# Optimization experiments

Hardware: AMD Instinct MI355X
Metric: run time of the kernel (lower is better)

Reference implementation:

```python
import jax, jax.numpy as jnp
import numpy as np

K = 3
TAPS = K ** 3  # 27 taps of the 3x3x3 kernel


def _conv3d(x, w, b):
    # x: (B,C,T,H,W), w: (O,I,kT,kH,kW), stride 1, pad 1
    y = jax.lax.conv_general_dilated(
        x, w, window_strides=(1, 1, 1),
        padding=((1, 1), (1, 1), (1, 1)),
        dimension_numbers=('NCDHW', 'OIDHW', 'NCDHW'))
    return y + b[None, :, None, None, None]


def _bilinear(xt, ph, pw):
    # xt: (B,C,T,H,W) temporally-shifted features; ph/pw: (B,T,H,W) float coords
    # zero padding outside the spatial extent (matches deform-conv semantics)
    B, C, T, H, W = xt.shape
    h0 = jnp.floor(ph)
    w0 = jnp.floor(pw)
    lh = (ph - h0)[:, None]  # (B,1,T,H,W)
    lw = (pw - w0)[:, None]
    h0i = h0.astype(jnp.int32)
    w0i = w0.astype(jnp.int32)
    xf = xt.reshape(B, C, T, H * W)

    def gather(hi, wi):
        valid = (hi >= 0) & (hi < H) & (wi >= 0) & (wi < W)
        idx = (jnp.clip(hi, 0, H - 1) * W + jnp.clip(wi, 0, W - 1)).reshape(B, 1, T, H * W)
        v = jnp.take_along_axis(xf, jnp.broadcast_to(idx, (B, C, T, H * W)), axis=3)
        return v.reshape(B, C, T, H, W) * valid[:, None].astype(xt.dtype)

    v00 = gather(h0i, w0i)
    v01 = gather(h0i, w0i + 1)
    v10 = gather(h0i + 1, w0i)
    v11 = gather(h0i + 1, w0i + 1)
    return (v00 * (1 - lh) * (1 - lw) + v01 * (1 - lh) * lw
            + v10 * lh * (1 - lw) + v11 * lh * lw)


def _dcn_hw(x, w_off, b_off, w, b):
    # DeformConvPack_d with dimension='HW': offsets deform H/W only, temporal taps rigid
    B, C, T, H, W = x.shape
    off = _conv3d(x, w_off, b_off).reshape(B, TAPS, 2, T, H, W)  # (dy, dx) per tap
    x_pad = jnp.pad(x, ((0, 0), (0, 0), (1, 1), (0, 0), (0, 0)))  # zero pad T
    hh = jnp.arange(H, dtype=x.dtype)[None, None, :, None]
    ww = jnp.arange(W, dtype=x.dtype)[None, None, None, :]
    out = jnp.zeros((B, w.shape[0], T, H, W), x.dtype)
    k = 0
    for kt in range(K):
        xt = x_pad[:, :, kt:kt + T]  # rigid temporal shift for this tap
        for kh in range(K):
            for kw in range(K):
                ph = hh + (kh - 1) + off[:, k, 0]
                pw = ww + (kw - 1) + off[:, k, 1]
                s = _bilinear(xt, ph, pw)  # (B,C,T,H,W)
                out = out + jnp.einsum('bcthw,oc->bothw', s, w[:, :, kt, kh, kw])
                k += 1
    return out + b[None, :, None, None, None]


def setup_inputs() -> dict:
    key = jax.random.key(0)
    ks = jax.random.split(key, 9)
    nf, B, T, H, W = 64, 1, 7, 96, 96
    sc = 1.0 / np.sqrt(nf * TAPS)
    return {
        'x': jax.random.normal(ks[0], (B, nf, T, H, W), jnp.float32),
        'w_off0': jax.random.normal(ks[1], (2 * TAPS, nf, K, K, K), jnp.float32) * 0.01,
        'b_off0': jax.random.normal(ks[2], (2 * TAPS,), jnp.float32) * 0.01,
        'w0': jax.random.normal(ks[3], (nf, nf, K, K, K), jnp.float32) * sc,
        'b0': jax.random.normal(ks[4], (nf,), jnp.float32) * 0.01,
        'w_off1': jax.random.normal(ks[5], (2 * TAPS, nf, K, K, K), jnp.float32) * 0.01,
        'b_off1': jax.random.normal(ks[6], (2 * TAPS,), jnp.float32) * 0.01,
        'w1': jax.random.normal(ks[7], (nf, nf, K, K, K), jnp.float32) * sc,
        'b1': jax.random.normal(ks[8], (nf,), jnp.float32) * 0.01,
    }


def reference(x, w_off0, b_off0, w0, b0, w_off1, b_off1, w1, b1):
    y = _dcn_hw(x, w_off0, b_off0, w0, b0)
    y = jnp.where(y > 0, y, 0.1 * y)  # LeakyReLU(0.1)
    return _dcn_hw(y, w_off1, b_off1, w1, b1) + x
```

## Files before the change

kernel.cpp:

```cpp
#include <hip/hip_runtime.h>
#include <hip/hip_fp16.h>

#define T_DIM 7
#define H_DIM 96
#define W_DIM 96
#define HW    (H_DIM*W_DIM)
#define L_DIM (T_DIM*HW)
#define NTAPS 27

#define TR 8
#define TC 16
#define HR (TR+8)
#define HC (TC+8)
#define HROWB (HC*128)
#define HALO_B (HR*HROWB)
#define WBUF_OFF HALO_B
#define SOFF_OFF (HALO_B + 16384)
#define SOFF_STRIDE 116
#define SMEM_B (SOFF_OFF + 128*SOFF_STRIDE)

typedef __attribute__((ext_vector_type(8))) _Float16 f16x8;
typedef __attribute__((ext_vector_type(4))) float f32x4;

#define GLOAD16(gp, lp) \
    __builtin_amdgcn_global_load_lds((const __attribute__((address_space(1))) unsigned int*)(gp), \
                                     (__attribute__((address_space(3))) unsigned int*)(lp), 16, 0, 0)

__global__ void prep_weights(const float* __restrict__ woff0,
                             const float* __restrict__ w0,
                             const float* __restrict__ woff1,
                             const float* __restrict__ w1,
                             unsigned short* __restrict__ dst)
{
    int idx = blockIdx.x * 256 + threadIdx.x;
    const int per = NTAPS * 64 * 64;
    if (idx >= 4 * per) return;
    int which = idx / per;
    int r     = idx % per;
    int tap   = r / 4096;
    int o     = (r >> 6) & 63;
    int c     = r & 63;
    const float* src = (which == 0) ? woff0 : (which == 1) ? w0
                     : (which == 2) ? woff1 : w1;
    int omax = (which == 0 || which == 2) ? 54 : 64;
    float v = 0.f;
    if (o < omax) v = src[(o * 64 + c) * NTAPS + tap];
    __half h = __float2half(v);
    int slot = (((c >> 3) + o) & 7);
    int pos  = tap * 4096 + o * 64 + slot * 8 + (c & 7);
    dst[which * per + pos] = __half_as_ushort(h);
}

__global__ void transpose_x(const float* __restrict__ x, unsigned* __restrict__ xt2)
{
    __shared__ float tile[64][65];
    const int tid = threadIdx.x;
    const int lb  = blockIdx.x * 64;
    const int ln  = tid & 63;
    const int q   = tid >> 6;
#pragma unroll
    for (int i = 0; i < 16; ++i) {
        int c = q + 4 * i;
        tile[ln][c] = x[(size_t)c * L_DIM + lb + ln];
    }
    __syncthreads();
    const int ln2 = tid & 31, q2 = tid >> 5;
#pragma unroll
    for (int i = 0; i < 8; ++i) {
        int ll = q2 + 8 * i;
        __half2 h2 = __float22half2_rn(make_float2(tile[ll][2*ln2], tile[ll][2*ln2+1]));
        xt2[(size_t)(lb + ll) * 32 + ln2] = *reinterpret_cast<unsigned*>(&h2);
    }
}

#define STAGE_SLAB(KT) { \
    int tp_ = t + (KT) - 1; \
    int tps_ = min(max(tp_, 0), T_DIM - 1); \
    const unsigned char* sb_ = xb + (size_t)tps_ * HW * 128; \
    _Pragma("unroll") \
    for (int i = 0; i < 6; ++i) { \
        int p16_ = tid + i * 512; \
        int hr_ = p16_ / 192; \
        int rem_ = p16_ - hr_ * 192; \
        int hc_ = rem_ >> 3; \
        int sl_ = rem_ & 7; \
        int ch_ = (sl_ - hc_) & 7; \
        int gr_ = min(max(row0 - 4 + hr_, 0), H_DIM - 1); \
        int gc_ = min(max(col0 - 4 + hc_, 0), W_DIM - 1); \
        GLOAD16(sb_ + (size_t)(gr_ * W_DIM + gc_) * 128 + ch_ * 16, \
                smem + (i << 13) + (wv << 10)); \
    } }

#define WSTAGE(WGBL, K) \
    GLOAD16((WGBL) + (size_t)(K) * 8192 + tid * 16, \
            smem + WBUF_OFF + (((K) & 1) << 13) + (wv << 10));

#define RUN_PHASE(DEF, WGBL) { \
    STAGE_SLAB(0); \
    WSTAGE(WGBL, 0); \
    asm volatile("s_waitcnt vmcnt(0)" ::: "memory"); \
    __builtin_amdgcn_s_barrier(); \
    __builtin_amdgcn_sched_barrier(0); \
    const unsigned char* soffp_ = smem + SOFF_OFF + (wv * 16 + lr) * SOFF_STRIDE; \
    float2 o2n_ = make_float2(0.f, 0.f); \
    if (DEF) { unsigned u_ = *(const unsigned*)(soffp_); \
               o2n_ = __half22float2(*reinterpret_cast<__half2*>(&u_)); } \
    _Pragma("unroll 1") \
    for (int kt = 0; kt < 3; ++kt) { \
        if (kt > 0) { \
            asm volatile("s_waitcnt lgkmcnt(0)" ::: "memory"); \
            __builtin_amdgcn_s_barrier();             \
            STAGE_SLAB(kt); \
            asm volatile("s_waitcnt vmcnt(0)" ::: "memory"); \
            __builtin_amdgcn_s_barrier(); \
            __builtin_amdgcn_sched_barrier(0); \
        } \
        int tp = t + kt - 1; \
        bool tv = (tp >= 0) && (tp < T_DIM); \
        _Pragma("unroll 1") \
        for (int k9 = 0; k9 < 9; ++k9) { \
            int k = kt * 9 + k9; \
            if (k > 0) { \
                asm volatile("s_waitcnt vmcnt(0) lgkmcnt(0)" ::: "memory");  \
                __builtin_amdgcn_s_barrier(); \
                __builtin_amdgcn_sched_barrier(0); \
            } \
            if (k + 1 < NTAPS) { WSTAGE(WGBL, k + 1); } \
            int kh = k9 / 3, kw = k9 - (k9 / 3) * 3; \
            f16x8 a0, a1; \
            if (DEF) { \
                float2 o2_ = o2n_; \
                if (k + 1 < NTAPS) { \
                    unsigned un_ = *(const unsigned*)(soffp_ + 4 * (k + 1)); \
                    o2n_ = __half22float2(*reinterpret_cast<__half2*>(&un_)); \
                } \
                float ph_ = (float)(row0 + wv + kh - 1) + o2_.x; \
                float pw_ = (float)(col0 + lr + kw - 1) + o2_.y; \
                float hf_ = floorf(ph_), wf_ = floorf(pw_); \
                float lh_ = ph_ - hf_, lw_ = pw_ - wf_; \
                int h0_ = (int)hf_, w0_ = (int)wf_; \
                __align__(16) __half2 va_[8]; \
                const __half2 z2_ = __float2half2_rn(0.f); \
                _Pragma("unroll") \
                for (int p = 0; p < 8; ++p) va_[p] = z2_; \
                _Pragma("unroll") \
                for (int j = 0; j < 4; ++j) { \
                    int hj_ = h0_ + (j >> 1), wj_ = w0_ + (j & 1); \
                    bool val_ = tv && (hj_ >= 0) && (hj_ < H_DIM) && (wj_ >= 0) && (wj_ < W_DIM); \
                    float wgt_ = ((j >> 1) ? lh_ : 1.f - lh_) * ((j & 1) ? lw_ : 1.f - lw_); \
                    __half2 cw_ = __float2half2_rn(val_ ? wgt_ : 0.f); \
                    int sr_ = min(max(hj_ - row0 + 4, 0), HR - 1); \
                    int sc_ = min(max(wj_ - col0 + 4, 0), HC - 1); \
                    const unsigned char* cell_ = smem + sr_ * HROWB + sc_ * 128; \
                    f16x8 c0_ = *(const f16x8*)(cell_ + (((lk + sc_) & 7) << 4)); \
                    f16x8 c1_ = *(const f16x8*)(cell_ + (((lk + 4 + sc_) & 7) << 4)); \
                    const __half2* p0_ = (const __half2*)&c0_; \
                    const __half2* p1_ = (const __half2*)&c1_; \
                    _Pragma("unroll") \
                    for (int d = 0; d < 4; ++d) { \
                        va_[d]     = __hfma2(p0_[d], cw_, va_[d]); \
                        va_[4 + d] = __hfma2(p1_[d], cw_, va_[4 + d]); \
                    } \
                } \
                a0 = *reinterpret_cast<f16x8*>(&va_[0]); \
                a1 = *reinterpret_cast<f16x8*>(&va_[4]); \
            } else { \
                int hj_ = row0 + wv + kh - 1, wj_ = col0 + lr + kw - 1; \
                bool val_ = tv && (hj_ >= 0) && (hj_ < H_DIM) && (wj_ >= 0) && (wj_ < W_DIM); \
                int sr_ = wv + kh + 3, sc_ = lr + kw + 3; \
                const unsigned char* cell_ = smem + sr_ * HROWB + sc_ * 128; \
                int4 z0_ = *(const int4*)(cell_ + (((lk + sc_) & 7) << 4)); \
                int4 z1_ = *(const int4*)(cell_ + (((lk + 4 + sc_) & 7) << 4)); \
                if (!val_) { z0_ = make_int4(0,0,0,0); z1_ = make_int4(0,0,0,0); } \
                a0 = *reinterpret_cast<f16x8*>(&z0_); \
                a1 = *reinterpret_cast<f16x8*>(&z1_); \
            } \
            const unsigned char* br_ = smem + WBUF_OFF + ((k & 1) << 13) + lr * 128; \
            _Pragma("unroll") \
            for (int n = 0; n < 4; ++n) { \
                f16x8 b0_ = *(const f16x8*)(br_ + n * 2048 + s0); \
                f16x8 b1_ = *(const f16x8*)(br_ + n * 2048 + s1); \
                acc[n] = __builtin_amdgcn_mfma_f32_16x16x32_f16(a0, b0_, acc[n], 0, 0, 0); \
                acc[n] = __builtin_amdgcn_mfma_f32_16x16x32_f16(a1, b1_, acc[n], 0, 0, 0); \
            } \
        } \
    } }

template<int EPI>
__global__ __launch_bounds__(512, 2)
void dcn_tile(const unsigned short* __restrict__ xin,
              const unsigned short* __restrict__ Wtoff,
              const unsigned short* __restrict__ Wtm,
              const float* __restrict__ boff,
              const float* __restrict__ bmain,
              const float* __restrict__ resid,
              float* __restrict__ outf,
              unsigned short* __restrict__ outh)
{
    __shared__ __align__(16) unsigned char smem[SMEM_B];

    const int tid  = threadIdx.x;
    const int wv   = tid >> 6, lane = tid & 63;
    const int lr   = lane & 15, lk = lane >> 4;

    const int bid = blockIdx.x;
    const int wg  = (bid & 7) * 63 + (bid >> 3);
    const int t   = wg / 72;
    const int rg  = (wg % 72) / 6;
    const int cg  = wg % 6;
    const int row0 = rg * TR;
    const int col0 = cg * TC;
    const int lrow = t * HW + (row0 + wv) * W_DIM + col0;

    const unsigned char* xb = (const unsigned char*)xin;

    const int s0 = ((lk + lr) & 7) << 4;
    const int s1 = ((lk + 4 + lr) & 7) << 4;

    f32x4 acc[4];
#pragma unroll
    for (int n = 0; n < 4; ++n) acc[n] = (f32x4){0.f, 0.f, 0.f, 0.f};

    RUN_PHASE(false, (const unsigned char*)Wtoff);

#pragma unroll
    for (int n = 0; n < 4; ++n) {
        int o = n * 16 + lr;
        if (o < 54) {
            float bvA = boff[o];
#pragma unroll
            for (int i = 0; i < 4; ++i) {
                int loc = wv * 16 + lk * 4 + i;
                float vv = acc[n][i] + bvA;
                *(unsigned short*)(smem + SOFF_OFF + loc * SOFF_STRIDE + o * 2) =
                    __half_as_ushort(__float2half(vv));
            }
        }
    }
    __syncthreads();

#pragma unroll
    for (int n = 0; n < 4; ++n) acc[n] = (f32x4){0.f, 0.f, 0.f, 0.f};

    RUN_PHASE(true, (const unsigned char*)Wtm);

    float bv[4];
#pragma unroll
    for (int n = 0; n < 4; ++n) bv[n] = bmain[n * 16 + lr];

    if (EPI == 1) {
#pragma unroll
        for (int n = 0; n < 4; ++n)
#pragma unroll
            for (int i = 0; i < 4; ++i) {
                int lc = lk * 4 + i;
                float vv = acc[n][i] + bv[n];
                vv = (vv > 0.f) ? vv : 0.1f * vv;
                outh[(size_t)(lrow + lc) * 64 + n * 16 + lr] =
                    __half_as_ushort(__float2half(vv));
            }
    } else {
        __syncthreads();
        float* tf = (float*)(smem + (wv << 12));
#pragma unroll
        for (int n = 0; n < 4; ++n)
#pragma unroll
            for (int i = 0; i < 4; ++i) {
                int lc = lk * 4 + i;
                int och = n * 16 + lr;
                tf[lc * 64 + ((och + 2 * lc) & 63)] = acc[n][i] + bv[n];
            }
        asm volatile("s_waitcnt lgkmcnt(0)" ::: "memory");
        __builtin_amdgcn_sched_barrier(0);
        int j = lane & 15, gq = lane >> 4;
#pragma unroll
        for (int it = 0; it < 16; ++it) {
            int och = gq * 16 + it;
            float val = tf[j * 64 + ((och + 2 * j) & 63)];
            size_t gi = (size_t)och * L_DIM + lrow + j;
            outf[gi] = val + resid[gi];
        }
    }
}

extern "C" void kernel_launch(void* const* d_in, const int* in_sizes, int n_in,
                              void* d_out, int out_size, void* d_ws, size_t ws_size,
                              hipStream_t stream)
{
    const float* x     = (const float*)d_in[0];
    const float* woff0 = (const float*)d_in[1];
    const float* boff0 = (const float*)d_in[2];
    const float* w0    = (const float*)d_in[3];
    const float* b0    = (const float*)d_in[4];
    const float* woff1 = (const float*)d_in[5];
    const float* boff1 = (const float*)d_in[6];
    const float* w1    = (const float*)d_in[7];
    const float* b1    = (const float*)d_in[8];
    float* out = (float*)d_out;

    unsigned char* ws = (unsigned char*)d_ws;
    unsigned short* Wt  = (unsigned short*)ws;
    unsigned short* xt  = (unsigned short*)(ws + 884736);
    unsigned short* y   = (unsigned short*)(ws + 9142272);

    prep_weights<<<1728, 256, 0, stream>>>(woff0, w0, woff1, w1, Wt);
    transpose_x<<<1008, 256, 0, stream>>>(x, (unsigned*)xt);

    const int grid = T_DIM * (H_DIM / TR) * (W_DIM / TC);
    const int WSZ  = NTAPS * 64 * 64;

    dcn_tile<1><<<grid, 512, 0, stream>>>(xt, Wt,           Wt + WSZ,     boff0, b0, nullptr, nullptr, y);
    dcn_tile<2><<<grid, 512, 0, stream>>>(y,  Wt + 2 * WSZ, Wt + 3 * WSZ, boff1, b1, x, out, nullptr);
}
```

Before: 129.2 us.

## Split channel reduction across wave pairs and load weights directly into registers

Each pair of waves now covers two output rows. The 64 input channels are split in half between the two waves of a pair, and the partial accumulators are combined through LDS after each phase. Weights are no longer staged into LDS; each lane loads its B fragments from global memory into registers, prefetching one tap ahead. This removes the per-tap barrier and weight LDS buffer, which cuts shared memory enough to raise launch bounds occupancy to 4. The cost is more global and L2 weight traffic, plus an extra reduction step with its own barriers.

```diff
diff --git a/kernel.cpp b/kernel.cpp
--- a/kernel.cpp
+++ b/kernel.cpp
@@ -14,9 +14,8 @@
 #define HC (TC+8)
 #define HROWB (HC*128)
 #define HALO_B (HR*HROWB)
-#define WBUF_OFF HALO_B
-#define SOFF_OFF (HALO_B + 16384)
-#define SOFF_STRIDE 116
+#define SOFF_OFF HALO_B
+#define SOFF_STRIDE 108
 #define SMEM_B (SOFF_OFF + 128*SOFF_STRIDE)
 
 typedef __attribute__((ext_vector_type(8))) _Float16 f16x8;
@@ -46,9 +45,7 @@
     float v = 0.f;
     if (o < omax) v = src[(o * 64 + c) * NTAPS + tap];
     __half h = __float2half(v);
-    int slot = (((c >> 3) + o) & 7);
-    int pos  = tap * 4096 + o * 64 + slot * 8 + (c & 7);
-    dst[which * per + pos] = __half_as_ushort(h);
+    dst[which * per + tap * 4096 + o * 64 + c] = __half_as_ushort(h);
 }
 
 __global__ void transpose_x(const float* __restrict__ x, unsigned* __restrict__ xt2)
@@ -91,25 +88,71 @@
                 smem + (i << 13) + (wv << 10)); \
     } }
 
-#define WSTAGE(WGBL, K) \
-    GLOAD16((WGBL) + (size_t)(K) * 8192 + tid * 16, \
-            smem + WBUF_OFF + (((K) & 1) << 13) + (wv << 10));
-
-#define RUN_PHASE(DEF, WGBL) { \
+#define BLOAD(WG, K, B0, B1, B2, B3) { \
+    const unsigned char* bp_ = (WG) + (size_t)(K) * 8192 + lr * 128 + kh2 * 64 + lk * 16; \
+    B0 = *(const int4*)(bp_);        B1 = *(const int4*)(bp_ + 2048); \
+    B2 = *(const int4*)(bp_ + 4096); B3 = *(const int4*)(bp_ + 6144); }
+
+#define READ_OFF(MT, K) ({ \
+    unsigned u_ = *(const unsigned*)(smem + SOFF_OFF + \
+        ((pair * 2 + (MT)) * 16 + lr) * SOFF_STRIDE + (K) * 4); \
+    __half22float2(*reinterpret_cast<__half2*>(&u_)); })
+
+#define GATHER_D(MT, O2, AV) { \
+    float ph_ = (float)(row0 + pair * 2 + (MT) + kh - 1) + (O2).x; \
+    float pw_ = (float)(col0 + lr + kw - 1) + (O2).y; \
+    float hf_ = floorf(ph_), wf_ = floorf(pw_); \
+    float lh_ = ph_ - hf_, lw_ = pw_ - wf_; \
+    int h0_ = (int)hf_, w0_ = (int)wf_; \
+    __align__(16) __half2 va_[4]; \
+    const __half2 z2_ = __float2half2_rn(0.f); \
+    va_[0] = z2_; va_[1] = z2_; va_[2] = z2_; va_[3] = z2_; \
+    _Pragma("unroll") \
+    for (int j = 0; j < 4; ++j) { \
+        int hj_ = h0_ + (j >> 1), wj_ = w0_ + (j & 1); \
+        bool v_ = tv && (hj_ >= 0) && (hj_ < H_DIM) && (wj_ >= 0) && (wj_ < W_DIM); \
+        float wg_ = ((j >> 1) ? lh_ : 1.f - lh_) * ((j & 1) ? lw_ : 1.f - lw_); \
+        __half2 cw_ = __float2half2_rn(v_ ? wg_ : 0.f); \
+        int sr_ = min(max(hj_ - row0 + 4, 0), HR - 1); \
+        int sc_ = min(max(wj_ - col0 + 4, 0), HC - 1); \
+        f16x8 c_ = *(const f16x8*)(smem + sr_ * HROWB + sc_ * 128 + \
+                                   (((kh2 * 4 + lk) + sc_) & 7) * 16); \
+        const __half2* p_ = (const __half2*)&c_; \
+        _Pragma("unroll") \
+        for (int d = 0; d < 4; ++d) va_[d] = __hfma2(p_[d], cw_, va_[d]); \
+    } \
+    AV = *reinterpret_cast<f16x8*>(&va_[0]); }
+
+#define GATHER_C(MT, AV) { \
+    int hj_ = row0 + pair * 2 + (MT) + kh - 1, wj_ = col0 + lr + kw - 1; \
+    bool v_ = tv && (hj_ >= 0) && (hj_ < H_DIM) && (wj_ >= 0) && (wj_ < W_DIM); \
+    int sr_ = pair * 2 + (MT) + kh + 3, sc_ = lr + kw + 3; \
+    int4 z_ = *(const int4*)(smem + sr_ * HROWB + sc_ * 128 + \
+                             (((kh2 * 4 + lk) + sc_) & 7) * 16); \
+    if (!v_) z_ = make_int4(0, 0, 0, 0); \
+    AV = *reinterpret_cast<f16x8*>(&z_); }
+
+#define MFMA_F16(A, B, C) __builtin_amdgcn_mfma_f32_16x16x32_f16( \
+    A, *reinterpret_cast<f16x8*>(&(B)), C, 0, 0, 0)
+
+#define RUN_PHASE(DEF, WGBLP) { \
+    const unsigned char* wgbl_ = (WGBLP); \
+    asm volatile("s_waitcnt lgkmcnt(0)" ::: "memory"); \
+    __builtin_amdgcn_s_barrier(); \
     STAGE_SLAB(0); \
-    WSTAGE(WGBL, 0); \
+    int4 b0, b1, b2, b3, n0, n1, n2, n3; \
+    BLOAD(wgbl_, 0, b0, b1, b2, b3); \
+    float2 oc0, oc1, on0, on1; \
+    oc0 = make_float2(0.f, 0.f); oc1 = oc0; on0 = oc0; on1 = oc0; \
+    if (DEF) { oc0 = READ_OFF(0, 0); oc1 = READ_OFF(1, 0); } \
     asm volatile("s_waitcnt vmcnt(0)" ::: "memory"); \
     __builtin_amdgcn_s_barrier(); \
     __builtin_amdgcn_sched_barrier(0); \
-    const unsigned char* soffp_ = smem + SOFF_OFF + (wv * 16 + lr) * SOFF_STRIDE; \
-    float2 o2n_ = make_float2(0.f, 0.f); \
-    if (DEF) { unsigned u_ = *(const unsigned*)(soffp_); \
-               o2n_ = __half22float2(*reinterpret_cast<__half2*>(&u_)); } \
     _Pragma("unroll 1") \
     for (int kt = 0; kt < 3; ++kt) { \
         if (kt > 0) { \
             asm volatile("s_waitcnt lgkmcnt(0)" ::: "memory"); \
-            __builtin_amdgcn_s_barrier();             \
+            __builtin_amdgcn_s_barrier(); \
             STAGE_SLAB(kt); \
             asm volatile("s_waitcnt vmcnt(0)" ::: "memory"); \
             __builtin_amdgcn_s_barrier(); \
@@ -120,88 +163,65 @@
         _Pragma("unroll 1") \
         for (int k9 = 0; k9 < 9; ++k9) { \
             int k = kt * 9 + k9; \
-            if (k > 0) { \
-                asm volatile("s_waitcnt vmcnt(0) lgkmcnt(0)" ::: "memory");  \
-                __builtin_amdgcn_s_barrier(); \
-                __builtin_amdgcn_sched_barrier(0); \
+            if (k + 1 < NTAPS) { \
+                BLOAD(wgbl_, k + 1, n0, n1, n2, n3); \
+                if (DEF) { on0 = READ_OFF(0, k + 1); on1 = READ_OFF(1, k + 1); } \
             } \
-            if (k + 1 < NTAPS) { WSTAGE(WGBL, k + 1); } \
             int kh = k9 / 3, kw = k9 - (k9 / 3) * 3; \
             f16x8 a0, a1; \
-            if (DEF) { \
-                float2 o2_ = o2n_; \
-                if (k + 1 < NTAPS) { \
-                    unsigned un_ = *(const unsigned*)(soffp_ + 4 * (k + 1)); \
-                    o2n_ = __half22float2(*reinterpret_cast<__half2*>(&un_)); \
-                } \
-                float ph_ = (float)(row0 + wv + kh - 1) + o2_.x; \
-                float pw_ = (float)(col0 + lr + kw - 1) + o2_.y; \
-                float hf_ = floorf(ph_), wf_ = floorf(pw_); \
-                float lh_ = ph_ - hf_, lw_ = pw_ - wf_; \
-                int h0_ = (int)hf_, w0_ = (int)wf_; \
-                __align__(16) __half2 va_[8]; \
-                const __half2 z2_ = __float2half2_rn(0.f); \
-                _Pragma("unroll") \
-                for (int p = 0; p < 8; ++p) va_[p] = z2_; \
-                _Pragma("unroll") \
-                for (int j = 0; j < 4; ++j) { \
-                    int hj_ = h0_ + (j >> 1), wj_ = w0_ + (j & 1); \
-                    bool val_ = tv && (hj_ >= 0) && (hj_ < H_DIM) && (wj_ >= 0) && (wj_ < W_DIM); \
-                    float wgt_ = ((j >> 1) ? lh_ : 1.f - lh_) * ((j & 1) ? lw_ : 1.f - lw_); \
-                    __half2 cw_ = __float2half2_rn(val_ ? wgt_ : 0.f); \
-                    int sr_ = min(max(hj_ - row0 + 4, 0), HR - 1); \
-                    int sc_ = min(max(wj_ - col0 + 4, 0), HC - 1); \
-                    const unsigned char* cell_ = smem + sr_ * HROWB + sc_ * 128; \
-                    f16x8 c0_ = *(const f16x8*)(cell_ + (((lk + sc_) & 7) << 4)); \
-                    f16x8 c1_ = *(const f16x8*)(cell_ + (((lk + 4 + sc_) & 7) << 4)); \
-                    const __half2* p0_ = (const __half2*)&c0_; \
-                    const __half2* p1_ = (const __half2*)&c1_; \
-                    _Pragma("unroll") \
-                    for (int d = 0; d < 4; ++d) { \
-                        va_[d]     = __hfma2(p0_[d], cw_, va_[d]); \
-                        va_[4 + d] = __hfma2(p1_[d], cw_, va_[4 + d]); \
-                    } \
-                } \
-                a0 = *reinterpret_cast<f16x8*>(&va_[0]); \
-                a1 = *reinterpret_cast<f16x8*>(&va_[4]); \
-            } else { \
-                int hj_ = row0 + wv + kh - 1, wj_ = col0 + lr + kw - 1; \
-                bool val_ = tv && (hj_ >= 0) && (hj_ < H_DIM) && (wj_ >= 0) && (wj_ < W_DIM); \
-                int sr_ = wv + kh + 3, sc_ = lr + kw + 3; \
-                const unsigned char* cell_ = smem + sr_ * HROWB + sc_ * 128; \
-                int4 z0_ = *(const int4*)(cell_ + (((lk + sc_) & 7) << 4)); \
-                int4 z1_ = *(const int4*)(cell_ + (((lk + 4 + sc_) & 7) << 4)); \
-                if (!val_) { z0_ = make_int4(0,0,0,0); z1_ = make_int4(0,0,0,0); } \
-                a0 = *reinterpret_cast<f16x8*>(&z0_); \
-                a1 = *reinterpret_cast<f16x8*>(&z1_); \
-            } \
-            const unsigned char* br_ = smem + WBUF_OFF + ((k & 1) << 13) + lr * 128; \
+            if (DEF) { GATHER_D(0, oc0, a0); GATHER_D(1, oc1, a1); } \
+            else     { GATHER_C(0, a0);      GATHER_C(1, a1); } \
+            acc[0][0] = MFMA_F16(a0, b0, acc[0][0]); \
+            acc[1][0] = MFMA_F16(a1, b0, acc[1][0]); \
+            acc[0][1] = MFMA_F16(a0, b1, acc[0][1]); \
+            acc[1][1] = MFMA_F16(a1, b1, acc[1][1]); \
+            acc[0][2] = MFMA_F16(a0, b2, acc[0][2]); \
+            acc[1][2] = MFMA_F16(a1, b2, acc[1][2]); \
+            acc[0][3] = MFMA_F16(a0, b3, acc[0][3]); \
+            acc[1][3] = MFMA_F16(a1, b3, acc[1][3]); \
+            b0 = n0; b1 = n1; b2 = n2; b3 = n3; \
+            oc0 = on0; oc1 = on1; \
+        } \
+    } }
+
+#define REDUCE_KSPLIT() { \
+    __syncthreads(); \
+    if (kh2 == 1) { \
+        _Pragma("unroll") \
+        for (int mt = 0; mt < 2; ++mt) \
+            _Pragma("unroll") \
+            for (int n = 0; n < 4; ++n) \
+                *(f32x4*)(smem + pair * 8192 + ((mt * 4 + n) << 10) + (lane << 4)) = acc[mt][n]; \
+    } \
+    __syncthreads(); \
+    if (kh2 == 0) { \
+        _Pragma("unroll") \
+        for (int mt = 0; mt < 2; ++mt) \
             _Pragma("unroll") \
             for (int n = 0; n < 4; ++n) { \
-                f16x8 b0_ = *(const f16x8*)(br_ + n * 2048 + s0); \
-                f16x8 b1_ = *(const f16x8*)(br_ + n * 2048 + s1); \
-                acc[n] = __builtin_amdgcn_mfma_f32_16x16x32_f16(a0, b0_, acc[n], 0, 0, 0); \
-                acc[n] = __builtin_amdgcn_mfma_f32_16x16x32_f16(a1, b1_, acc[n], 0, 0, 0); \
+                f32x4 o_ = *(const f32x4*)(smem + pair * 8192 + ((mt * 4 + n) << 10) + (lane << 4)); \
+                acc[mt][n] += o_; \
             } \
-        } \
     } }
 
 template<int EPI>
-__global__ __launch_bounds__(512, 2)
-void dcn_tile(const unsigned short* __restrict__ xin,
-              const unsigned short* __restrict__ Wtoff,
-              const unsigned short* __restrict__ Wtm,
-              const float* __restrict__ boff,
-              const float* __restrict__ bmain,
-              const float* __restrict__ resid,
-              float* __restrict__ outf,
-              unsigned short* __restrict__ outh)
+__global__ __launch_bounds__(512, 4)
+void dcn_ks(const unsigned short* __restrict__ xin,
+            const unsigned short* __restrict__ Wtoff,
+            const unsigned short* __restrict__ Wtm,
+            const float* __restrict__ boff,
+            const float* __restrict__ bmain,
+            const float* __restrict__ resid,
+            float* __restrict__ outf,
+            unsigned short* __restrict__ outh)
 {
     __shared__ __align__(16) unsigned char smem[SMEM_B];
 
     const int tid  = threadIdx.x;
     const int wv   = tid >> 6, lane = tid & 63;
     const int lr   = lane & 15, lk = lane >> 4;
+    const int pair = wv >> 1;
+    const int kh2  = wv & 1;
 
     const int bid = blockIdx.x;
     const int wg  = (bid & 7) * 63 + (bid >> 3);
@@ -210,39 +230,45 @@
     const int cg  = wg % 6;
     const int row0 = rg * TR;
     const int col0 = cg * TC;
-    const int lrow = t * HW + (row0 + wv) * W_DIM + col0;
 
     const unsigned char* xb = (const unsigned char*)xin;
 
-    const int s0 = ((lk + lr) & 7) << 4;
-    const int s1 = ((lk + 4 + lr) & 7) << 4;
-
-    f32x4 acc[4];
-#pragma unroll
-    for (int n = 0; n < 4; ++n) acc[n] = (f32x4){0.f, 0.f, 0.f, 0.f};
+    f32x4 acc[2][4];
+#pragma unroll
+    for (int mt = 0; mt < 2; ++mt)
+#pragma unroll
+        for (int n = 0; n < 4; ++n) acc[mt][n] = (f32x4){0.f, 0.f, 0.f, 0.f};
 
     RUN_PHASE(false, (const unsigned char*)Wtoff);
-
-#pragma unroll
-    for (int n = 0; n < 4; ++n) {
-        int o = n * 16 + lr;
-        if (o < 54) {
-            float bvA = boff[o];
-#pragma unroll
-            for (int i = 0; i < 4; ++i) {
-                int loc = wv * 16 + lk * 4 + i;
-                float vv = acc[n][i] + bvA;
-                *(unsigned short*)(smem + SOFF_OFF + loc * SOFF_STRIDE + o * 2) =
-                    __half_as_ushort(__float2half(vv));
+    REDUCE_KSPLIT();
+    if (kh2 == 0) {
+#pragma unroll
+        for (int n = 0; n < 4; ++n) {
+            int o = n * 16 + lr;
+            if (o < 54) {
+                float bvA = boff[o];
+#pragma unroll
+                for (int mt = 0; mt < 2; ++mt)
+#pragma unroll
+                    for (int i = 0; i < 4; ++i) {
+                        int l = (pair * 2 + mt) * 16 + lk * 4 + i;
+                        float vv = acc[mt][n][i] + bvA;
+                        *(unsigned short*)(smem + SOFF_OFF + l * SOFF_STRIDE + o * 2) =
+                            __half_as_ushort(__float2half(vv));
+                    }
             }
         }
     }
     __syncthreads();
 
 #pragma unroll
-    for (int n = 0; n < 4; ++n) acc[n] = (f32x4){0.f, 0.f, 0.f, 0.f};
+    for (int mt = 0; mt < 2; ++mt)
+#pragma unroll
+        for (int n = 0; n < 4; ++n) acc[mt][n] = (f32x4){0.f, 0.f, 0.f, 0.f};
 
     RUN_PHASE(true, (const unsigned char*)Wtm);
+    REDUCE_KSPLIT();
+    if (kh2 == 1) return;
 
     float bv[4];
 #pragma unroll
@@ -250,35 +276,45 @@
 
     if (EPI == 1) {
 #pragma unroll
-        for (int n = 0; n < 4; ++n)
-#pragma unroll
-            for (int i = 0; i < 4; ++i) {
-                int lc = lk * 4 + i;
-                float vv = acc[n][i] + bv[n];
-                vv = (vv > 0.f) ? vv : 0.1f * vv;
-                outh[(size_t)(lrow + lc) * 64 + n * 16 + lr] =
-                    __half_as_ushort(__float2half(vv));
-            }
+        for (int mt = 0; mt < 2; ++mt) {
+            size_t lrowmt = (size_t)t * HW + (size_t)(row0 + pair * 2 + mt) * W_DIM + col0;
+#pragma unroll
+            for (int n = 0; n < 4; ++n)
+#pragma unroll
+                for (int i = 0; i < 4; ++i) {
+                    int lc = lk * 4 + i;
+                    float vv = acc[mt][n][i] + bv[n];
+                    vv = (vv > 0.f) ? vv : 0.1f * vv;
+                    outh[(lrowmt + lc) * 64 + n * 16 + lr] =
+                        __half_as_ushort(__float2half(vv));
+                }
+        }
     } else {
-        __syncthreads();
-        float* tf = (float*)(smem + (wv << 12));
-#pragma unroll
-        for (int n = 0; n < 4; ++n)
-#pragma unroll
-            for (int i = 0; i < 4; ++i) {
-                int lc = lk * 4 + i;
-                int och = n * 16 + lr;
-                tf[lc * 64 + ((och + 2 * lc) & 63)] = acc[n][i] + bv[n];
-            }
+        float* tf = (float*)(smem + pair * 8192);
+#pragma unroll
+        for (int mt = 0; mt < 2; ++mt)
+#pragma unroll
+            for (int n = 0; n < 4; ++n)
+#pragma unroll
+                for (int i = 0; i < 4; ++i) {
+                    int l = mt * 16 + lk * 4 + i;
+                    int och = n * 16 + lr;
+                    tf[l * 64 + ((och + 2 * l) & 63)] = acc[mt][n][i] + bv[n];
+                }
         asm volatile("s_waitcnt lgkmcnt(0)" ::: "memory");
         __builtin_amdgcn_sched_barrier(0);
         int j = lane & 15, gq = lane >> 4;
 #pragma unroll
-        for (int it = 0; it < 16; ++it) {
-            int och = gq * 16 + it;
-            float val = tf[j * 64 + ((och + 2 * j) & 63)];
-            size_t gi = (size_t)och * L_DIM + lrow + j;
-            outf[gi] = val + resid[gi];
+        for (int mt = 0; mt < 2; ++mt) {
+            size_t lrowmt = (size_t)t * HW + (size_t)(row0 + pair * 2 + mt) * W_DIM + col0;
+#pragma unroll
+            for (int it = 0; it < 16; ++it) {
+                int och = gq * 16 + it;
+                int l = mt * 16 + j;
+                float val = tf[l * 64 + ((och + 2 * l) & 63)];
+                size_t gi = (size_t)och * L_DIM + lrowmt + j;
+                outf[gi] = val + resid[gi];
+            }
         }
     }
 }
@@ -309,6 +345,6 @@
     const int grid = T_DIM * (H_DIM / TR) * (W_DIM / TC);
     const int WSZ  = NTAPS * 64 * 64;
 
-    dcn_tile<1><<<grid, 512, 0, stream>>>(xt, Wt,           Wt + WSZ,     boff0, b0, nullptr, nullptr, y);
-    dcn_tile<2><<<grid, 512, 0, stream>>>(y,  Wt + 2 * WSZ, Wt + 3 * WSZ, boff1, b1, x, out, nullptr);
+    dcn_ks<1><<<grid, 512, 0, stream>>>(xt, Wt,           Wt + WSZ,     boff0, b0, nullptr, nullptr, y);
+    dcn_ks<2><<<grid, 512, 0, stream>>>(y,  Wt + 2 * WSZ, Wt + 3 * WSZ, boff1, b1, x, out, nullptr);
 }
```

After: 235.5 us. +82.2%, slower.
